# Kernel tuning notes

Measured on AMD Instinct MI355X. Metric: run time of the kernel, lower is better.

The kernel has to match this reference:

```python
import jax, jax.numpy as jnp
import numpy as np

B, S, SE, D, H, FF, E, K = 2, 2048, 2048, 1024, 16, 4096, 8, 2
HD = D // H


def setup_inputs() -> dict:
    key = jax.random.key(0)
    ks = jax.random.split(key, 32)
    w = lambda k, shape: jax.random.normal(k, shape, jnp.float32) * 0.02
    inp = {
        'x': jax.random.normal(ks[0], (B, S, D), jnp.float32),
        'encoder_output': jax.random.normal(ks[1], (B, SE, D), jnp.float32),
        # causal self-attention projections
        'sa_wq': w(ks[2], (D, D)), 'sa_bq': jnp.zeros((D,), jnp.float32),
        'sa_wk': w(ks[3], (D, D)), 'sa_bk': jnp.zeros((D,), jnp.float32),
        'sa_wv': w(ks[4], (D, D)), 'sa_bv': jnp.zeros((D,), jnp.float32),
        'sa_wo': w(ks[5], (D, D)), 'sa_bo': jnp.zeros((D,), jnp.float32),
        # cross-attention projections
        'ca_wq': w(ks[6], (D, D)), 'ca_bq': jnp.zeros((D,), jnp.float32),
        'ca_wk': w(ks[7], (D, D)), 'ca_bk': jnp.zeros((D,), jnp.float32),
        'ca_wv': w(ks[8], (D, D)), 'ca_bv': jnp.zeros((D,), jnp.float32),
        'ca_wo': w(ks[9], (D, D)), 'ca_bo': jnp.zeros((D,), jnp.float32),
        # layernorms
        'ln1_g': jnp.ones((D,), jnp.float32), 'ln1_b': jnp.zeros((D,), jnp.float32),
        'ln2_g': jnp.ones((D,), jnp.float32), 'ln2_b': jnp.zeros((D,), jnp.float32),
        'ln3_g': jnp.ones((D,), jnp.float32), 'ln3_b': jnp.zeros((D,), jnp.float32),
        # router + experts
        'router_w': w(ks[10], (D, E)), 'router_b': jnp.zeros((E,), jnp.float32),
        'e_w1': w(ks[11], (E, D, FF)), 'e_b1': jnp.zeros((E, FF), jnp.float32),
        'e_w2': w(ks[12], (E, FF, D)), 'e_b2': jnp.zeros((E, D), jnp.float32),
    }
    return inp


def _layernorm(x, g, b):
    m = x.mean(-1, keepdims=True)
    v = ((x - m) ** 2).mean(-1, keepdims=True)
    return (x - m) / jnp.sqrt(v + 1e-5) * g + b


def _attn(q_in, k_in, v_in, wq, bq, wk, bk, wv, bv, wo, bo, causal):
    Bq, Sq, Dm = q_in.shape
    Sk = k_in.shape[1]
    Q = (q_in @ wq + bq).reshape(Bq, Sq, H, HD)
    Kp = (k_in @ wk + bk).reshape(Bq, Sk, H, HD)
    V = (v_in @ wv + bv).reshape(Bq, Sk, H, HD)
    scores = jnp.einsum('bqhd,bkhd->bhqk', Q, Kp) / jnp.sqrt(jnp.float32(HD))
    if causal:
        mask = jnp.tril(jnp.ones((Sq, Sk), bool))
        scores = jnp.where(mask, scores, -jnp.inf)
    a = jax.nn.softmax(scores, axis=-1)
    o = jnp.einsum('bhqk,bkhd->bqhd', a, V).reshape(Bq, Sq, Dm)
    return o @ wo + bo


def _moe(x, rw, rb, w1, b1, w2, b2):
    T = x.shape[0] * x.shape[1]
    xf = x.reshape(T, D)
    router_weights = jax.nn.softmax(xf @ rw + rb, axis=-1)          # [T,E]
    topw, topi = jax.lax.top_k(router_weights, K)                   # [T,K]
    topw = jax.nn.softmax(topw, axis=-1)                            # renormalize top-k
    # combine[t,e] = sum_k topw[t,k] * (topi[t,k]==e)
    combine = jnp.zeros((T, E), xf.dtype).at[jnp.arange(T)[:, None], topi].add(topw)
    # dense compute over all experts (same math as masked dispatch)
    h = jax.nn.gelu(jnp.einsum('td,edf->etf', xf, w1) + b1[:, None, :], approximate=False)
    eo = jnp.einsum('etf,efd->etd', h, w2) + b2[:, None, :]          # [E,T,D]
    out = jnp.einsum('etd,te->td', eo, combine)
    return out.reshape(x.shape)


def reference(x, encoder_output,
              sa_wq, sa_bq, sa_wk, sa_bk, sa_wv, sa_bv, sa_wo, sa_bo,
              ca_wq, ca_bq, ca_wk, ca_bk, ca_wv, ca_bv, ca_wo, ca_bo,
              ln1_g, ln1_b, ln2_g, ln2_b, ln3_g, ln3_b,
              router_w, router_b, e_w1, e_b1, e_w2, e_b2):
    x = _layernorm(x + _attn(x, x, x, sa_wq, sa_bq, sa_wk, sa_bk, sa_wv, sa_bv, sa_wo, sa_bo, True), ln1_g, ln1_b)
    x = _layernorm(x + _attn(x, encoder_output, encoder_output, ca_wq, ca_bq, ca_wk, ca_bk, ca_wv, ca_bv, ca_wo, ca_bo, False), ln2_g, ln2_b)
    x = _layernorm(x + _moe(x, router_w, router_b, e_w1, e_b1, e_w2, e_b2), ln3_g, ln3_b)
    return x
```

## Files before the change

kernel.cpp:

```cpp
#include <hip/hip_runtime.h>

typedef unsigned short u16;
typedef unsigned int   u32;
typedef __bf16    bf16x8 __attribute__((ext_vector_type(8)));
typedef _Float16  f16x8  __attribute__((ext_vector_type(8)));
typedef _Float16  f16x4  __attribute__((ext_vector_type(4)));
typedef __fp16    fp16x2 __attribute__((ext_vector_type(2)));
typedef float     f32x4  __attribute__((ext_vector_type(4)));
typedef u16       u16x4  __attribute__((ext_vector_type(4)));

#define DEV static __device__ __forceinline__

#if __has_builtin(__builtin_amdgcn_mfma_f32_16x16x16f16)
#define HAVE_MFMA16 1
#else
#define HAVE_MFMA16 0
#endif

constexpr int DIMc  = 1024;
constexpr int NHEAD = 16;
constexpr int HDM   = 64;
constexpr int SLENc = 2048;
constexpr int NBAT  = 2;
constexpr int NTOK  = NBAT * SLENc;
constexpr int FFD   = 4096;
constexpr int NEXP  = 8;
constexpr int NSLOT = 2 * NTOK;
constexpr long TD   = (long)NTOK * DIMc;
constexpr float RSC = 2048.0f;
constexpr float RSCI = 1.0f / 2048.0f;

DEV u16 f2bf(float f) {
  u32 u = __float_as_uint(f);
  u += 0x7fffu + ((u >> 16) & 1u);
  return (u16)(u >> 16);
}
DEV float bf2f(u16 h) { return __uint_as_float(((u32)h) << 16); }
DEV float h2f(u16 u) { union { _Float16 h; u16 u_; } x; x.u_ = u; return (float)x.h; }

DEV void split2v(float v, u16& h, u16& r) {
  _Float16 hh = (_Float16)v;
  float rf = (v - (float)hh) * RSC;
  union { _Float16 h_; u16 u_; } a, b;
  a.h_ = hh; b.h_ = (_Float16)rf;
  h = a.u_; r = b.u_;
}

DEV u32 pkrtz(float a, float b) {
  union { fp16x2 v; u32 u; } x;
  x.v = __builtin_amdgcn_cvt_pkrtz(a, b);
  return x.u;
}

DEV f16x4 mk4(u32 lo, u32 hi) {
  union { u32 u[2]; f16x4 v; } x;
  x.u[0] = lo; x.u[1] = hi;
  return x.v;
}

DEV void async16(const void* g, void* l) {
  __builtin_amdgcn_global_load_lds((const u32*)g, (u32*)l, 16, 0, 0);
}

DEV f32x4 mfma_bf(bf16x8 a, bf16x8 b, f32x4 c) {
  return __builtin_amdgcn_mfma_f32_16x16x32_bf16(a, b, c, 0, 0, 0);
}
DEV f32x4 mfma_h(f16x8 a, f16x8 b, f32x4 c) {
  return __builtin_amdgcn_mfma_f32_16x16x32_f16(a, b, c, 0, 0, 0);
}
#if HAVE_MFMA16
DEV f32x4 mfma16h(f16x4 a, f16x4 b, f32x4 c) {
  return __builtin_amdgcn_mfma_f32_16x16x16f16(a, b, c, 0, 0, 0);
}
#endif

DEV f16x8 ldfragh(const u16 (*T)[64], int row, int blk) {
  return *(const f16x8*)((const u16*)T + row * 64 + ((blk ^ (row & 7)) * 8));
}
DEV f16x4 ldVfrag4(const u16 (*T)[64], int row, int kn, int kc) {
  const int blk = kn * 2 + (kc >> 1);
  const u16* p = (const u16*)T + row * 64 + ((blk ^ (row & 7)) * 8) + (kc & 1) * 4;
  return *(const f16x4*)p;
}

DEV float gelu_fast(float v) {
  float arg = v * fmaf(0.044715f * v, v, 1.0f) * 0.7978845608028654f;
  return v / (1.0f + __expf(-2.0f * arg));
}

__global__ __launch_bounds__(256) void split2_kernel(
    const float* __restrict__ x, u16* __restrict__ o0, u16* __restrict__ o1, long n) {
  long i = ((long)blockIdx.x * 256 + threadIdx.x) * 4;
  if (i >= n) return;
  f32x4 v = *(const f32x4*)(x + i);
  u16x4 h, r;
#pragma unroll
  for (int j = 0; j < 4; ++j) { u16 a, b; split2v(v[j], a, b); h[j] = a; r[j] = b; }
  *(u16x4*)(o0 + i) = h;
  *(u16x4*)(o1 + i) = r;
}

__global__ __launch_bounds__(256) void wsplit2_kernel(
    const float* __restrict__ W, u16* __restrict__ t0, u16* __restrict__ t1, int R, int C) {
  __shared__ alignas(16) float tile[32][33];
  const long base = (long)blockIdx.z * R * C;
  const int c0 = blockIdx.x * 32, r0 = blockIdx.y * 32;
  const int tx = threadIdx.x & 31, ty = threadIdx.x >> 5;
#pragma unroll
  for (int i = 0; i < 32; i += 8)
    tile[ty + i][tx] = W[base + (long)(r0 + ty + i) * C + (c0 + tx)];
  __syncthreads();
#pragma unroll
  for (int i = 0; i < 32; i += 8) {
    float v = tile[tx][ty + i];
    long oidx = base + (long)(c0 + ty + i) * R + (r0 + tx);
    u16 a, b; split2v(v, a, b);
    t0[oidx] = a; t1[oidx] = b;
  }
}

__global__ __launch_bounds__(256) void wsplit1_kernel(
    const float* __restrict__ W, u16* __restrict__ t0, int R, int C) {
  __shared__ alignas(16) float tile[32][33];
  const long base = (long)blockIdx.z * R * C;
  const int c0 = blockIdx.x * 32, r0 = blockIdx.y * 32;
  const int tx = threadIdx.x & 31, ty = threadIdx.x >> 5;
#pragma unroll
  for (int i = 0; i < 32; i += 8)
    tile[ty + i][tx] = W[base + (long)(r0 + ty + i) * C + (c0 + tx)];
  __syncthreads();
#pragma unroll
  for (int i = 0; i < 32; i += 8) {
    long oidx = base + (long)(c0 + ty + i) * R + (r0 + tx);
    t0[oidx] = f2bf(tile[tx][ty + i]);
  }
}

__global__ __launch_bounds__(256) void biascat_kernel(
    const float* __restrict__ q, const float* __restrict__ k, const float* __restrict__ v,
    const float* __restrict__ ck, const float* __restrict__ cv,
    float* __restrict__ qkvb, float* __restrict__ kvb) {
  int i = blockIdx.x * 256 + threadIdx.x;
  if (i < 1024) qkvb[i] = q[i];
  else if (i < 2048) qkvb[i] = k[i - 1024];
  else if (i < 3072) qkvb[i] = v[i - 2048];
  else if (i < 4096) kvb[i - 3072] = ck[i - 3072];
  else if (i < 5120) kvb[i - 3072] = cv[i - 4096];
}

__global__ __launch_bounds__(256) void vtrans2_kernel(
    const u16* __restrict__ vh, const u16* __restrict__ vr, int ld,
    u16* __restrict__ t0, u16* __restrict__ t1) {
  __shared__ alignas(16) float tile[32][33];
  const int bh = blockIdx.z, b = bh >> 4, h = bh & 15;
  const int s0 = blockIdx.x * 32, d0 = blockIdx.y * 32;
  const int tx = threadIdx.x & 31, ty = threadIdx.x >> 5;
#pragma unroll
  for (int i = 0; i < 32; i += 8) {
    long idx = (long)(b * SLENc + s0 + ty + i) * ld + h * HDM + d0 + tx;
    tile[ty + i][tx] = h2f(vh[idx]) + h2f(vr[idx]) * RSCI;
  }
  __syncthreads();
#pragma unroll
  for (int i = 0; i < 32; i += 8) {
    float v = tile[tx][ty + i];
    long o = ((long)bh * HDM + d0 + ty + i) * SLENc + s0 + tx;
    u16 a, b_; split2v(v, a, b_);
    t0[o] = a; t1[o] = b_;
  }
}

template<int MT, int BK, bool SPLIT, bool GATHER, int EPI>
__global__ __launch_bounds__(256) void gemm_kernel(
    const u16* __restrict__ A0, const u16* __restrict__ A1,
    const u16* __restrict__ B0, const u16* __restrict__ B1,
    const float* __restrict__ bias, void* __restrict__ Cout, u16* __restrict__ C1,
    int M, int N, int Kd,
    const int* __restrict__ tlist, const int* __restrict__ cnts, const int* __restrict__ offs) {
  constexpr int NP   = SPLIT ? 2 : 1;
  constexpr int RPC  = 512 / BK;
  constexpr int ACH  = (MT / RPC) / 4;
  constexpr int BCH  = (128 / RPC) / 4;
  constexpr int MREP = MT / 32;
  constexpr int WRS  = MT / 2;
  __shared__ alignas(16) u16 As[NP][MT * BK];
  __shared__ alignas(16) u16 Bs[NP][128 * BK];

  const int e   = blockIdx.z;
  const int cnt = cnts ? cnts[e] : M;
  const int off = offs ? offs[e] : 0;
  const int m0  = blockIdx.y * MT;
  if (m0 >= cnt) return;
  const int n0  = blockIdx.x * 128;

  const int tid = threadIdx.x;
  const int lane = tid & 63, wid = tid >> 6;
  const int fr = lane & 15, kc = lane >> 4;
  const int wr = wid >> 1, wc = wid & 1;

  const long boff = (long)e * N * Kd;

  int srow, kseg8;
  if constexpr (BK == 32) { srow = lane >> 2; kseg8 = lane & 3; }
  else                    { srow = lane >> 3; kseg8 = (lane & 7) ^ (srow & 7); }

  long aoff[ACH], boff_[BCH];
#pragma unroll
  for (int c = 0; c < ACH; ++c) {
    const int row = (wid * ACH + c) * RPC + srow;
    long ar;
    if (GATHER) {
      int idx = m0 + row; if (idx >= cnt) idx = cnt - 1;
      ar = tlist[off + idx];
    } else {
      ar = (long)(off + m0 + row);
    }
    aoff[c] = ar * Kd + kseg8 * 8;
  }
#pragma unroll
  for (int c = 0; c < BCH; ++c) {
    const int row = (wid * BCH + c) * RPC + srow;
    boff_[c] = boff + (long)(n0 + row) * Kd + kseg8 * 8;
  }

  f32x4 acc[MREP][4], acc1[MREP][4];
#pragma unroll
  for (int m = 0; m < MREP; ++m)
#pragma unroll
    for (int n = 0; n < 4; ++n) { acc[m][n] = f32x4{0.f,0.f,0.f,0.f}; acc1[m][n] = f32x4{0.f,0.f,0.f,0.f}; }

  const int NK = Kd / BK;
  for (int kt = 0; kt < NK; ++kt) {
    const int k0 = kt * BK;
    __syncthreads();
#pragma unroll
    for (int c = 0; c < ACH; ++c) {
      const int chunk = wid * ACH + c;
      async16(A0 + aoff[c] + k0, &As[0][chunk * 512]);
      if constexpr (SPLIT) async16(A1 + aoff[c] + k0, &As[1][chunk * 512]);
    }
#pragma unroll
    for (int c = 0; c < BCH; ++c) {
      const int chunk = wid * BCH + c;
      async16(B0 + boff_[c] + k0, &Bs[0][chunk * 512]);
      if constexpr (SPLIT) async16(B1 + boff_[c] + k0, &Bs[1][chunk * 512]);
    }
    __syncthreads();

    if constexpr (BK == 32) {
      if constexpr (SPLIT) {
        f16x8 a0[MREP], a1[MREP];
#pragma unroll
        for (int m = 0; m < MREP; ++m) {
          const int idx = (wr * WRS + m * 16 + fr) * 32 + kc * 8;
          a0[m] = *(const f16x8*)&As[0][idx];
          a1[m] = *(const f16x8*)&As[1][idx];
        }
#pragma unroll
        for (int n = 0; n < 4; ++n) {
          const int idx = (wc * 64 + n * 16 + fr) * 32 + kc * 8;
          f16x8 b0 = *(const f16x8*)&Bs[0][idx];
          f16x8 b1 = *(const f16x8*)&Bs[1][idx];
#pragma unroll
          for (int m = 0; m < MREP; ++m) {
            acc[m][n]  = mfma_h(a0[m], b0, acc[m][n]);
            acc1[m][n] = mfma_h(a0[m], b1, acc1[m][n]);
            acc1[m][n] = mfma_h(a1[m], b0, acc1[m][n]);
          }
        }
      } else {
        bf16x8 a0[MREP];
#pragma unroll
        for (int m = 0; m < MREP; ++m)
          a0[m] = *(const bf16x8*)&As[0][(wr * WRS + m * 16 + fr) * 32 + kc * 8];
#pragma unroll
        for (int n = 0; n < 4; ++n) {
          bf16x8 b0 = *(const bf16x8*)&Bs[0][(wc * 64 + n * 16 + fr) * 32 + kc * 8];
#pragma unroll
          for (int m = 0; m < MREP; ++m)
            acc[m][n] = mfma_bf(a0[m], b0, acc[m][n]);
        }
      }
    } else {
#pragma unroll
      for (int ksub = 0; ksub < 2; ++ksub) {
        bf16x8 a0[MREP];
#pragma unroll
        for (int m = 0; m < MREP; ++m) {
          const int row = wr * WRS + m * 16 + fr;
          a0[m] = *(const bf16x8*)&As[0][row * 64 + (((ksub << 2) | kc) ^ (fr & 7)) * 8];
        }
#pragma unroll
        for (int n = 0; n < 4; ++n) {
          const int row = wc * 64 + n * 16 + fr;
          bf16x8 b0 = *(const bf16x8*)&Bs[0][row * 64 + (((ksub << 2) | kc) ^ (fr & 7)) * 8];
#pragma unroll
          for (int m = 0; m < MREP; ++m)
            acc[m][n] = mfma_bf(a0[m], b0, acc[m][n]);
        }
      }
    }
  }

  const float* bvec = bias + (long)e * N;
#pragma unroll
  for (int m = 0; m < MREP; ++m) {
#pragma unroll
    for (int j = 0; j < 4; ++j) {
      const int r = m0 + wr * WRS + m * 16 + kc * 4 + j;
      if (r >= cnt) continue;
      const long orow = (long)(off + r) * N;
#pragma unroll
      for (int n = 0; n < 4; ++n) {
        const int col = n0 + wc * 64 + n * 16 + fr;
        float v = acc[m][n][j];
        if constexpr (SPLIT) v += acc1[m][n][j] * RSCI;
        v += bvec[col];
        if constexpr (EPI == 0) {
          ((float*)Cout)[orow + col] = v;
        } else if constexpr (EPI == 1) {
          ((u16*)Cout)[orow + col] = f2bf(gelu_fast(v));
        } else if constexpr (EPI == 2) {
          ((u16*)Cout)[orow + col] = f2bf(v);
        } else {
          u16 a_, b_; split2v(v, a_, b_);
          ((u16*)Cout)[orow + col] = a_;
          C1[orow + col] = b_;
        }
      }
    }
  }
}

#if !HAVE_MFMA16
DEV f16x8 gather_fragh(u32 a0, u32 a1, u32 b0, u32 b1, int lane) {
  const int kc = lane >> 4;
  const int base = (lane & 15) + ((kc & 1) << 5);
  union { u32 u[4]; f16x8 v; } r;
  u32 s00 = (u32)__shfl((int)a0, base, 64);
  u32 s01 = (u32)__shfl((int)a1, base, 64);
  u32 s10 = (u32)__shfl((int)b0, base, 64);
  u32 s11 = (u32)__shfl((int)b1, base, 64);
  u32 t00 = (u32)__shfl((int)a0, base + 16, 64);
  u32 t01 = (u32)__shfl((int)a1, base + 16, 64);
  u32 t10 = (u32)__shfl((int)b0, base + 16, 64);
  u32 t11 = (u32)__shfl((int)b1, base + 16, 64);
  const bool hi = (kc >> 1) != 0;
  r.u[0] = hi ? s10 : s00;
  r.u[1] = hi ? s11 : s01;
  r.u[2] = hi ? t10 : t00;
  r.u[3] = hi ? t11 : t01;
  return r.v;
}
#endif

template<bool CAUSAL>
__global__ __launch_bounds__(256, 3) void attn2_kernel(
    const u16* __restrict__ Qh, const u16* __restrict__ Qr, int qld,
    const u16* __restrict__ Kh, const u16* __restrict__ Kr, int kld,
    const u16* __restrict__ Vh, const u16* __restrict__ Vr,
    u16* __restrict__ OH, u16* __restrict__ OR) {
  __shared__ alignas(16) u16 KQs[2][64][64];
  __shared__ alignas(16) u16 Vts[2][64][64];

  const int qt = CAUSAL ? ((int)gridDim.x - 1 - (int)blockIdx.x) : (int)blockIdx.x;
  const int h = blockIdx.y, b = blockIdx.z;
  const int tid = threadIdx.x, lane = tid & 63, w = tid >> 6;
  const int fr = lane & 15, kc = lane >> 4;
  const int q0 = qt * 64;
  const long qbase = (long)(b * SLENc) * qld + h * HDM;
  const long kbase = (long)(b * SLENc) * kld + h * HDM;
  const long obase = (long)(b * SLENc) * DIMc + h * HDM;
  const long vtbase = (long)(b * NHEAD + h) * HDM * SLENc;
  const int r = lane >> 3, blk = (lane & 7) ^ r;

#pragma unroll
  for (int p = 0; p < 2; ++p) {
    const u16* gp = (p == 0 ? Qh : Qr);
#pragma unroll
    for (int cc = 0; cc < 2; ++cc) {
      int c = w + 4 * cc;
      async16(gp + qbase + (long)(q0 + 8 * c + r) * qld + blk * 8, &KQs[p][8 * c][0]);
    }
  }
  __syncthreads();
  f16x8 qf0[2], qf1[2];
#pragma unroll
  for (int s = 0; s < 2; ++s) {
    qf0[s] = ldfragh(KQs[0], w * 16 + fr, s * 4 + kc);
    qf1[s] = ldfragh(KQs[1], w * 16 + fr, s * 4 + kc);
  }
  __syncthreads();

  f32x4 accO0[4], accO1[4];
#pragma unroll
  for (int dn = 0; dn < 4; ++dn) { accO0[dn] = f32x4{0.f,0.f,0.f,0.f}; accO1[dn] = f32x4{0.f,0.f,0.f,0.f}; }
  float m_ = -3e38f, l_ = 0.f;

  const int nkt = CAUSAL ? (qt + 1) : (SLENc / 64);
  for (int kt = 0; kt < nkt; ++kt) {
    __syncthreads();
    {
#pragma unroll
      for (int p = 0; p < 2; ++p) {
        const u16* gp = (p == 0 ? Kh : Kr);
#pragma unroll
        for (int cc = 0; cc < 2; ++cc) {
          int c = w + 4 * cc;
          async16(gp + kbase + (long)(kt * 64 + 8 * c + r) * kld + blk * 8, &KQs[p][8 * c][0]);
        }
      }
      const long vrow = vtbase + kt * 64;
#pragma unroll
      for (int p = 0; p < 2; ++p) {
        const u16* gp = (p == 0 ? Vh : Vr);
#pragma unroll
        for (int cc = 0; cc < 2; ++cc) {
          int c = w + 4 * cc;
          async16(gp + vrow + (long)(8 * c + r) * SLENc + blk * 8, &Vts[p][8 * c][0]);
        }
      }
    }
    __syncthreads();

    f32x4 sc0[4], sc1[4];
#pragma unroll
    for (int kn = 0; kn < 4; ++kn) { sc0[kn] = f32x4{0.f,0.f,0.f,0.f}; sc1[kn] = f32x4{0.f,0.f,0.f,0.f}; }
    __builtin_amdgcn_s_setprio(1);
#pragma unroll
    for (int kn = 0; kn < 4; ++kn)
#pragma unroll
      for (int s = 0; s < 2; ++s) {
        f16x8 ah = ldfragh(KQs[0], kn * 16 + fr, s * 4 + kc);
        f16x8 ar = ldfragh(KQs[1], kn * 16 + fr, s * 4 + kc);
        sc0[kn] = mfma_h(ah, qf0[s], sc0[kn]);
        sc1[kn] = mfma_h(ah, qf1[s], sc1[kn]);
        sc1[kn] = mfma_h(ar, qf0[s], sc1[kn]);
      }
    __builtin_amdgcn_s_setprio(0);

    constexpr float SCL = 0.125f, SCL2 = 0.125f * RSCI;
    float p_[4][4];
    float mx = -3e38f;
#pragma unroll
    for (int kn = 0; kn < 4; ++kn)
#pragma unroll
      for (int j = 0; j < 4; ++j) {
        float sv = fmaf(sc0[kn][j], SCL, sc1[kn][j] * SCL2);
        if (CAUSAL && kt == qt) {
          if (kn * 16 + kc * 4 + j > w * 16 + fr) sv = -3e38f;
        }
        p_[kn][j] = sv;
        mx = fmaxf(mx, sv);
      }
    mx = fmaxf(mx, __shfl_xor(mx, 16, 64));
    mx = fmaxf(mx, __shfl_xor(mx, 32, 64));
    if (!__all(mx <= m_ + 8.f)) {
      const float mn = fmaxf(m_, mx);
      const float corr = __expf(m_ - mn);
      m_ = mn;
      l_ *= corr;
#pragma unroll
      for (int dn = 0; dn < 4; ++dn) { accO0[dn] *= corr; accO1[dn] *= corr; }
    }
    float rs = 0.f;
#pragma unroll
    for (int kn = 0; kn < 4; ++kn)
#pragma unroll
      for (int j = 0; j < 4; ++j) {
        float p = __expf(p_[kn][j] - m_);
        p_[kn][j] = p;
        rs += p;
      }
    rs += __shfl_xor(rs, 16, 64);
    rs += __shfl_xor(rs, 32, 64);
    l_ += rs;

#if HAVE_MFMA16
#pragma unroll
    for (int kn = 0; kn < 4; ++kn) {
      u32 hp0 = pkrtz(p_[kn][0], p_[kn][1]);
      u32 hp1 = pkrtz(p_[kn][2], p_[kn][3]);
      float h0 = h2f((u16)hp0), h1 = h2f((u16)(hp0 >> 16));
      float h2_ = h2f((u16)hp1), h3 = h2f((u16)(hp1 >> 16));
      u32 rp0 = pkrtz((p_[kn][0] - h0) * RSC, (p_[kn][1] - h1) * RSC);
      u32 rp1 = pkrtz((p_[kn][2] - h2_) * RSC, (p_[kn][3] - h3) * RSC);
      f16x4 ph = mk4(hp0, hp1), pr = mk4(rp0, rp1);
      __builtin_amdgcn_s_setprio(1);
#pragma unroll
      for (int dn = 0; dn < 4; ++dn) {
        f16x4 vh = ldVfrag4(Vts[0], dn * 16 + fr, kn, kc);
        f16x4 vr = ldVfrag4(Vts[1], dn * 16 + fr, kn, kc);
        accO0[dn] = mfma16h(vh, ph, accO0[dn]);
        accO1[dn] = mfma16h(vh, pr, accO1[dn]);
        accO1[dn] = mfma16h(vr, ph, accO1[dn]);
      }
      __builtin_amdgcn_s_setprio(0);
    }
#else
    u32 hpk[4][2], rpk[4][2];
#pragma unroll
    for (int kn = 0; kn < 4; ++kn)
#pragma unroll
      for (int jp = 0; jp < 2; ++jp) {
        float p0 = p_[kn][2 * jp], p1 = p_[kn][2 * jp + 1];
        u32 hp = pkrtz(p0, p1);
        float h0 = h2f((u16)hp), h1 = h2f((u16)(hp >> 16));
        u32 rp = pkrtz((p0 - h0) * RSC, (p1 - h1) * RSC);
        hpk[kn][jp] = hp;
        rpk[kn][jp] = rp;
      }
#pragma unroll
    for (int s = 0; s < 2; ++s) {
      f16x8 ph = gather_fragh(hpk[2 * s][0], hpk[2 * s][1], hpk[2 * s + 1][0], hpk[2 * s + 1][1], lane);
      f16x8 pr = gather_fragh(rpk[2 * s][0], rpk[2 * s][1], rpk[2 * s + 1][0], rpk[2 * s + 1][1], lane);
      __builtin_amdgcn_s_setprio(1);
#pragma unroll
      for (int dn = 0; dn < 4; ++dn) {
        f16x8 vh = ldfragh(Vts[0], dn * 16 + fr, s * 4 + kc);
        f16x8 vr = ldfragh(Vts[1], dn * 16 + fr, s * 4 + kc);
        accO0[dn] = mfma_h(vh, ph, accO0[dn]);
        accO1[dn] = mfma_h(vh, pr, accO1[dn]);
        accO1[dn] = mfma_h(vr, ph, accO1[dn]);
      }
      __builtin_amdgcn_s_setprio(0);
    }
#endif
  }

  const float inv = 1.0f / l_;
#pragma unroll
  for (int dn = 0; dn < 4; ++dn) {
    u16x4 hv, rv;
#pragma unroll
    for (int j = 0; j < 4; ++j) {
      float o = (accO0[dn][j] + accO1[dn][j] * RSCI) * inv;
      u16 a_, b_; split2v(o, a_, b_);
      hv[j] = a_; rv[j] = b_;
    }
    const long oidx = obase + (long)(q0 + w * 16 + fr) * DIMc + dn * 16 + kc * 4;
    *(u16x4*)&OH[oidx] = hv;
    *(u16x4*)&OR[oidx] = rv;
  }
}

template<int NS>
__global__ __launch_bounds__(256) void resln_kernel(
    const float* __restrict__ resid, const float* __restrict__ proj,
    const float* __restrict__ gam, const float* __restrict__ bet,
    float* __restrict__ yout, u16* __restrict__ s0, u16* __restrict__ s1) {
  __shared__ float red[4];
  const int t = blockIdx.x, tid = threadIdx.x;
  const long base = (long)t * DIMc;
  float v[4];
#pragma unroll
  for (int i = 0; i < 4; ++i) {
    int d = tid + i * 256;
    v[i] = resid[base + d] + proj[base + d];
  }
  float s = v[0] + v[1] + v[2] + v[3];
#pragma unroll
  for (int o = 32; o; o >>= 1) s += __shfl_xor(s, o, 64);
  if ((tid & 63) == 0) red[tid >> 6] = s;
  __syncthreads();
  const float mean = (red[0] + red[1] + red[2] + red[3]) * (1.0f / DIMc);
  __syncthreads();
  float q = 0.f;
#pragma unroll
  for (int i = 0; i < 4; ++i) { float d_ = v[i] - mean; q += d_ * d_; }
#pragma unroll
  for (int o = 32; o; o >>= 1) q += __shfl_xor(q, o, 64);
  if ((tid & 63) == 0) red[tid >> 6] = q;
  __syncthreads();
  const float var = (red[0] + red[1] + red[2] + red[3]) * (1.0f / DIMc);
  const float inv = rsqrtf(var + 1e-5f);
#pragma unroll
  for (int i = 0; i < 4; ++i) {
    int d = tid + i * 256;
    float y = (v[i] - mean) * inv * gam[d] + bet[d];
    yout[base + d] = y;
    if constexpr (NS == 1) s0[base + d] = f2bf(y);
    if constexpr (NS == 2) {
      u16 a, b; split2v(y, a, b);
      s0[base + d] = a; s1[base + d] = b;
    }
  }
}

__global__ __launch_bounds__(256) void resln_router_kernel(
    const float* __restrict__ resid, const float* __restrict__ proj,
    const float* __restrict__ gam, const float* __restrict__ bet,
    const float* __restrict__ rw, const float* __restrict__ rb,
    float* __restrict__ yout, u16* __restrict__ s0,
    int* __restrict__ topi, float* __restrict__ topw, int* __restrict__ cnt) {
  __shared__ float red[4];
  __shared__ float rpart[4][8];
  const int t = blockIdx.x, tid = threadIdx.x;
  const int lane = tid & 63, wv = tid >> 6;
  const long base = (long)t * DIMc;
  float v[4];
#pragma unroll
  for (int i = 0; i < 4; ++i) {
    int d = tid + i * 256;
    v[i] = resid[base + d] + proj[base + d];
  }
  float s = v[0] + v[1] + v[2] + v[3];
#pragma unroll
  for (int o = 32; o; o >>= 1) s += __shfl_xor(s, o, 64);
  if (lane == 0) red[wv] = s;
  __syncthreads();
  const float mean = (red[0] + red[1] + red[2] + red[3]) * (1.0f / DIMc);
  __syncthreads();
  float q = 0.f;
#pragma unroll
  for (int i = 0; i < 4; ++i) { float d_ = v[i] - mean; q += d_ * d_; }
#pragma unroll
  for (int o = 32; o; o >>= 1) q += __shfl_xor(q, o, 64);
  if (lane == 0) red[wv] = q;
  __syncthreads();
  const float var = (red[0] + red[1] + red[2] + red[3]) * (1.0f / DIMc);
  const float inv = rsqrtf(var + 1e-5f);
  float part[8] = {};
#pragma unroll
  for (int i = 0; i < 4; ++i) {
    int d = tid + i * 256;
    float y = (v[i] - mean) * inv * gam[d] + bet[d];
    yout[base + d] = y;
    s0[base + d] = f2bf(y);
    const f32x4* wp = (const f32x4*)&rw[d * 8];
    f32x4 w0 = wp[0], w1 = wp[1];
    part[0] += y * w0[0]; part[1] += y * w0[1]; part[2] += y * w0[2]; part[3] += y * w0[3];
    part[4] += y * w1[0]; part[5] += y * w1[1]; part[6] += y * w1[2]; part[7] += y * w1[3];
  }
#pragma unroll
  for (int o = 32; o; o >>= 1)
#pragma unroll
    for (int e = 0; e < 8; ++e) part[e] += __shfl_xor(part[e], o, 64);
  if (lane == 0)
#pragma unroll
    for (int e = 0; e < 8; ++e) rpart[wv][e] = part[e];
  __syncthreads();
  if (tid == 0) {
    float lg[8];
#pragma unroll
    for (int e = 0; e < 8; ++e)
      lg[e] = rpart[0][e] + rpart[1][e] + rpart[2][e] + rpart[3][e] + rb[e];
    int i1 = 0;
#pragma unroll
    for (int e = 1; e < 8; ++e) if (lg[e] > lg[i1]) i1 = e;
    int i2 = (i1 == 0) ? 1 : 0;
#pragma unroll
    for (int e = 0; e < 8; ++e) if (e != i1 && lg[e] > lg[i2]) i2 = e;
    float mx = lg[i1], ps = 0.f, p[8];
#pragma unroll
    for (int e = 0; e < 8; ++e) { p[e] = __expf(lg[e] - mx); ps += p[e]; }
    float p1 = p[i1] / ps, p2 = p[i2] / ps;
    float e2 = __expf(p2 - p1);
    float w1 = 1.0f / (1.0f + e2);
    topi[t * 2] = i1; topi[t * 2 + 1] = i2;
    topw[t * 2] = w1; topw[t * 2 + 1] = e2 * w1;
    atomicAdd(&cnt[i1], 1); atomicAdd(&cnt[i2], 1);
  }
}

__global__ void scan_kernel(const int* __restrict__ cnt, int* __restrict__ offs, int* __restrict__ pos) {
  if (threadIdx.x == 0) {
    int a = 0;
    for (int e = 0; e < NEXP; ++e) { offs[e] = a; a += cnt[e]; }
  }
  if (threadIdx.x < NEXP) pos[threadIdx.x] = 0;
}

__global__ __launch_bounds__(256) void fill_kernel(
    const int* __restrict__ topi, const int* __restrict__ offs, int* __restrict__ pos,
    int* __restrict__ tlist, int* __restrict__ slotof) {
  int t = blockIdx.x * 256 + threadIdx.x;
  if (t >= NTOK) return;
#pragma unroll
  for (int k = 0; k < 2; ++k) {
    int e = topi[t * 2 + k];
    int pp = atomicAdd(&pos[e], 1);
    int s = offs[e] + pp;
    tlist[s] = t;
    slotof[t * 2 + k] = s;
  }
}

__global__ __launch_bounds__(256) void final_kernel(
    const float* __restrict__ x2, const u16* __restrict__ eo,
    const int* __restrict__ slotof, const float* __restrict__ topw,
    const float* __restrict__ gam, const float* __restrict__ bet, float* __restrict__ out) {
  __shared__ float red[4];
  const int t = blockIdx.x, tid = threadIdx.x;
  const long base = (long)t * DIMc;
  const int s0 = slotof[t * 2], s1 = slotof[t * 2 + 1];
  const float w0 = topw[t * 2], w1 = topw[t * 2 + 1];
  float v[4];
#pragma unroll
  for (int i = 0; i < 4; ++i) {
    int d = tid + i * 256;
    float moe = w0 * bf2f(eo[(long)s0 * DIMc + d]) + w1 * bf2f(eo[(long)s1 * DIMc + d]);
    v[i] = x2[base + d] + moe;
  }
  float s = v[0] + v[1] + v[2] + v[3];
#pragma unroll
  for (int o = 32; o; o >>= 1) s += __shfl_xor(s, o, 64);
  if ((tid & 63) == 0) red[tid >> 6] = s;
  __syncthreads();
  const float mean = (red[0] + red[1] + red[2] + red[3]) * (1.0f / DIMc);
  __syncthreads();
  float q = 0.f;
#pragma unroll
  for (int i = 0; i < 4; ++i) { float d_ = v[i] - mean; q += d_ * d_; }
#pragma unroll
  for (int o = 32; o; o >>= 1) q += __shfl_xor(q, o, 64);
  if ((tid & 63) == 0) red[tid >> 6] = q;
  __syncthreads();
  const float var = (red[0] + red[1] + red[2] + red[3]) * (1.0f / DIMc);
  const float inv = rsqrtf(var + 1e-5f);
#pragma unroll
  for (int i = 0; i < 4; ++i) {
    int d = tid + i * 256;
    out[base + d] = (v[i] - mean) * inv * gam[d] + bet[d];
  }
}

extern "C" void kernel_launch(void* const* d_in, const int* in_sizes, int n_in,
                              void* d_out, int out_size, void* d_ws, size_t ws_size,
                              hipStream_t stream) {
  (void)in_sizes; (void)n_in; (void)out_size; (void)ws_size;
  const float* x     = (const float*)d_in[0];
  const float* enc   = (const float*)d_in[1];
  const float* aw[8] = {(const float*)d_in[2],  (const float*)d_in[4],  (const float*)d_in[6],  (const float*)d_in[8],
                        (const float*)d_in[10], (const float*)d_in[12], (const float*)d_in[14], (const float*)d_in[16]};
  const float* ab[8] = {(const float*)d_in[3],  (const float*)d_in[5],  (const float*)d_in[7],  (const float*)d_in[9],
                        (const float*)d_in[11], (const float*)d_in[13], (const float*)d_in[15], (const float*)d_in[17]};
  const float* ln1_g = (const float*)d_in[18]; const float* ln1_b = (const float*)d_in[19];
  const float* ln2_g = (const float*)d_in[20]; const float* ln2_b = (const float*)d_in[21];
  const float* ln3_g = (const float*)d_in[22]; const float* ln3_b = (const float*)d_in[23];
  const float* rw    = (const float*)d_in[24]; const float* rb    = (const float*)d_in[25];
  const float* e_w1  = (const float*)d_in[26]; const float* e_b1  = (const float*)d_in[27];
  const float* e_w2  = (const float*)d_in[28]; const float* e_b2  = (const float*)d_in[29];

  char* basep = (char*)d_ws;
  size_t offb = 0;
  auto alloc = [&](size_t nbytes) -> void* {
    void* r = basep + offb;
    offb += (nbytes + 255) & ~(size_t)255;
    return r;
  };

  const size_t PLANE_BF = (size_t)TD * 2;
  const size_t PLANE_F  = (size_t)TD * 4;
  const size_t WPLANE   = (size_t)DIMc * DIMc * 2;

  u16 *xs0 = (u16*)alloc(PLANE_BF), *xs1 = (u16*)alloc(PLANE_BF);
  u16 *es0 = (u16*)alloc(PLANE_BF), *es1 = (u16*)alloc(PLANE_BF);
  u16 *os0 = (u16*)alloc(PLANE_BF), *os1 = (u16*)alloc(PLANE_BF);
  u16 *wqkv0 = (u16*)alloc(3 * WPLANE), *wqkv1 = (u16*)alloc(3 * WPLANE);
  u16 *wkv0  = (u16*)alloc(2 * WPLANE), *wkv1  = (u16*)alloc(2 * WPLANE);
  u16 *wq0   = (u16*)alloc(WPLANE),     *wq1   = (u16*)alloc(WPLANE);
  u16 *wo10  = (u16*)alloc(WPLANE),     *wo11  = (u16*)alloc(WPLANE);
  u16 *wo20  = (u16*)alloc(WPLANE),     *wo21  = (u16*)alloc(WPLANE);
  u16* w1t = (u16*)alloc((size_t)NEXP * FFD * DIMc * 2);
  u16* w2t = (u16*)alloc((size_t)NEXP * DIMc * FFD * 2);
  u16 *QKVh = (u16*)alloc(3 * PLANE_BF), *QKVr = (u16*)alloc(3 * PLANE_BF);
  u16 *KVh  = (u16*)alloc(2 * PLANE_BF), *KVr  = (u16*)alloc(2 * PLANE_BF);
  u16 *Qch  = (u16*)alloc(PLANE_BF),     *Qcr  = (u16*)alloc(PLANE_BF);
  u16 *Vth  = (u16*)alloc(PLANE_BF),     *Vtr  = (u16*)alloc(PLANE_BF);
  float* qkvb = (float*)alloc(3072 * 4);
  float* kvb  = (float*)alloc(2048 * 4);
  float* aout = (float*)alloc(PLANE_F);
  float* x1   = (float*)alloc(PLANE_F);
  float* x2   = (float*)alloc(PLANE_F);
  u16*   x2h  = (u16*)alloc(PLANE_BF);
  u16*   hbuf = (u16*)alloc((size_t)(NSLOT + 128) * FFD * 2);
  u16*   eo   = (u16*)alloc((size_t)NSLOT * DIMc * 2);
  int*   topi   = (int*)alloc(NSLOT * 4);
  float* topwp  = (float*)alloc(NSLOT * 4);
  int*   tlist  = (int*)alloc(NSLOT * 4);
  int*   slotof = (int*)alloc(NSLOT * 4);
  int*   cnt    = (int*)alloc(NEXP * 4);
  int*   offs   = (int*)alloc(NEXP * 4);
  int*   pos    = (int*)alloc(NEXP * 4);

  (void)hipMemsetAsync(cnt, 0, NEXP * sizeof(int), stream);

  const int SB = (int)(TD / 4 / 256);
  split2_kernel<<<SB, 256, 0, stream>>>(x, xs0, xs1, TD);
  split2_kernel<<<SB, 256, 0, stream>>>(enc, es0, es1, TD);
  for (int s = 0; s < 3; ++s)
    wsplit2_kernel<<<dim3(32, 32, 1), 256, 0, stream>>>(aw[s], wqkv0 + (size_t)s * DIMc * DIMc, wqkv1 + (size_t)s * DIMc * DIMc, DIMc, DIMc);
  wsplit2_kernel<<<dim3(32, 32, 1), 256, 0, stream>>>(aw[5], wkv0, wkv1, DIMc, DIMc);
  wsplit2_kernel<<<dim3(32, 32, 1), 256, 0, stream>>>(aw[6], wkv0 + (size_t)DIMc * DIMc, wkv1 + (size_t)DIMc * DIMc, DIMc, DIMc);
  wsplit2_kernel<<<dim3(32, 32, 1), 256, 0, stream>>>(aw[4], wq0, wq1, DIMc, DIMc);
  wsplit2_kernel<<<dim3(32, 32, 1), 256, 0, stream>>>(aw[3], wo10, wo11, DIMc, DIMc);
  wsplit2_kernel<<<dim3(32, 32, 1), 256, 0, stream>>>(aw[7], wo20, wo21, DIMc, DIMc);
  wsplit1_kernel<<<dim3(FFD / 32, DIMc / 32, NEXP), 256, 0, stream>>>(e_w1, w1t, DIMc, FFD);
  wsplit1_kernel<<<dim3(DIMc / 32, FFD / 32, NEXP), 256, 0, stream>>>(e_w2, w2t, FFD, DIMc);
  biascat_kernel<<<20, 256, 0, stream>>>(ab[0], ab[1], ab[2], ab[5], ab[6], qkvb, kvb);

  const dim3 gproj(DIMc / 128, NTOK / 64, 1);
  const dim3 gqkv(3 * DIMc / 128, NTOK / 64, 1);
  const dim3 gkv(2 * DIMc / 128, NTOK / 64, 1);
  const dim3 gattn(SLENc / 64, NHEAD, NBAT);
  const dim3 gvt(SLENc / 32, HDM / 32, NBAT * NHEAD);

  gemm_kernel<64, 32, true, false, 3><<<gqkv, 256, 0, stream>>>(xs0, xs1, wqkv0, wqkv1, qkvb, QKVh, QKVr, NTOK, 3 * DIMc, DIMc, nullptr, nullptr, nullptr);
  vtrans2_kernel<<<gvt, 256, 0, stream>>>(QKVh + 2048, QKVr + 2048, 3 * DIMc, Vth, Vtr);
  attn2_kernel<true><<<gattn, 256, 0, stream>>>(QKVh, QKVr, 3 * DIMc, QKVh + 1024, QKVr + 1024, 3 * DIMc, Vth, Vtr, os0, os1);
  gemm_kernel<64, 32, true, false, 0><<<gproj, 256, 0, stream>>>(os0, os1, wo10, wo11, ab[3], aout, nullptr, NTOK, DIMc, DIMc, nullptr, nullptr, nullptr);
  resln_kernel<2><<<NTOK, 256, 0, stream>>>(x, aout, ln1_g, ln1_b, x1, xs0, xs1);
  gemm_kernel<64, 32, true, false, 3><<<gproj, 256, 0, stream>>>(xs0, xs1, wq0, wq1, ab[4], Qch, Qcr, NTOK, DIMc, DIMc, nullptr, nullptr, nullptr);
  gemm_kernel<64, 32, true, false, 3><<<gkv, 256, 0, stream>>>(es0, es1, wkv0, wkv1, kvb, KVh, KVr, NTOK, 2 * DIMc, DIMc, nullptr, nullptr, nullptr);
  vtrans2_kernel<<<gvt, 256, 0, stream>>>(KVh + 1024, KVr + 1024, 2 * DIMc, Vth, Vtr);
  attn2_kernel<false><<<gattn, 256, 0, stream>>>(Qch, Qcr, DIMc, KVh, KVr, 2 * DIMc, Vth, Vtr, os0, os1);
  gemm_kernel<64, 32, true, false, 0><<<gproj, 256, 0, stream>>>(os0, os1, wo20, wo21, ab[7], aout, nullptr, NTOK, DIMc, DIMc, nullptr, nullptr, nullptr);
  resln_router_kernel<<<NTOK, 256, 0, stream>>>(x1, aout, ln2_g, ln2_b, rw, rb, x2, x2h, topi, topwp, cnt);
  scan_kernel<<<1, 64, 0, stream>>>(cnt, offs, pos);
  fill_kernel<<<NTOK / 256, 256, 0, stream>>>(topi, offs, pos, tlist, slotof);
  gemm_kernel<128, 64, false, true, 1><<<dim3(FFD / 128, NTOK / 128, NEXP), 256, 0, stream>>>(
      x2h, nullptr, w1t, nullptr, e_b1, hbuf, nullptr, NTOK, FFD, DIMc, tlist, cnt, offs);
  gemm_kernel<128, 64, false, false, 2><<<dim3(DIMc / 128, NTOK / 128, NEXP), 256, 0, stream>>>(
      hbuf, nullptr, w2t, nullptr, e_b2, eo, nullptr, NTOK, DIMc, FFD, nullptr, cnt, offs);
  final_kernel<<<NTOK, 256, 0, stream>>>(x2, eo, slotof, topwp, ln3_g, ln3_b, (float*)d_out);
}
```

Before: 1.201 ms.

## Double-buffer shared-memory tiles in GEMM and attention to overlap loads with MFMA

The BK=32 GEMM path and the attention kernel now use two shared-memory buffers. The next K/V (or A/B) tile is issued asynchronously right after the barrier, and the MFMA work runs on the current buffer, removing one barrier per iteration and hiding global-load latency behind compute. The cost is double the LDS footprint in the attention kernel, whose launch bound drops from 3 to 2 blocks per CU, and more LDS in the GEMM. That can reduce occupancy.

After: 1.187 ms. About the same (-1.2%).

```diff
diff --git a/kernel.cpp b/kernel.cpp
--- a/kernel.cpp
+++ b/kernel.cpp
@@ -178,13 +178,14 @@
     int M, int N, int Kd,
     const int* __restrict__ tlist, const int* __restrict__ cnts, const int* __restrict__ offs) {
   constexpr int NP   = SPLIT ? 2 : 1;
+  constexpr int NBUF = (BK == 32) ? 2 : 1;
   constexpr int RPC  = 512 / BK;
   constexpr int ACH  = (MT / RPC) / 4;
   constexpr int BCH  = (128 / RPC) / 4;
   constexpr int MREP = MT / 32;
   constexpr int WRS  = MT / 2;
-  __shared__ alignas(16) u16 As[NP][MT * BK];
-  __shared__ alignas(16) u16 Bs[NP][128 * BK];
+  __shared__ alignas(16) u16 As[NBUF][NP][MT * BK];
+  __shared__ alignas(16) u16 Bs[NBUF][NP][128 * BK];
 
   const int e   = blockIdx.z;
   const int cnt = cnts ? cnts[e] : M;
@@ -229,38 +230,37 @@
 #pragma unroll
     for (int n = 0; n < 4; ++n) { acc[m][n] = f32x4{0.f,0.f,0.f,0.f}; acc1[m][n] = f32x4{0.f,0.f,0.f,0.f}; }
 
-  const int NK = Kd / BK;
-  for (int kt = 0; kt < NK; ++kt) {
+  auto stage = [&](int kt, int bufi) {
     const int k0 = kt * BK;
-    __syncthreads();
 #pragma unroll
     for (int c = 0; c < ACH; ++c) {
       const int chunk = wid * ACH + c;
-      async16(A0 + aoff[c] + k0, &As[0][chunk * 512]);
-      if constexpr (SPLIT) async16(A1 + aoff[c] + k0, &As[1][chunk * 512]);
+      async16(A0 + aoff[c] + k0, &As[bufi][0][chunk * 512]);
+      if constexpr (SPLIT) async16(A1 + aoff[c] + k0, &As[bufi][1][chunk * 512]);
     }
 #pragma unroll
     for (int c = 0; c < BCH; ++c) {
       const int chunk = wid * BCH + c;
-      async16(B0 + boff_[c] + k0, &Bs[0][chunk * 512]);
-      if constexpr (SPLIT) async16(B1 + boff_[c] + k0, &Bs[1][chunk * 512]);
-    }
-    __syncthreads();
-
+      async16(B0 + boff_[c] + k0, &Bs[bufi][0][chunk * 512]);
+      if constexpr (SPLIT) async16(B1 + boff_[c] + k0, &Bs[bufi][1][chunk * 512]);
+    }
+  };
+
+  auto compute = [&](int bufi) {
     if constexpr (BK == 32) {
       if constexpr (SPLIT) {
         f16x8 a0[MREP], a1[MREP];
 #pragma unroll
         for (int m = 0; m < MREP; ++m) {
           const int idx = (wr * WRS + m * 16 + fr) * 32 + kc * 8;
-          a0[m] = *(const f16x8*)&As[0][idx];
-          a1[m] = *(const f16x8*)&As[1][idx];
+          a0[m] = *(const f16x8*)&As[bufi][0][idx];
+          a1[m] = *(const f16x8*)&As[bufi][1][idx];
         }
 #pragma unroll
         for (int n = 0; n < 4; ++n) {
           const int idx = (wc * 64 + n * 16 + fr) * 32 + kc * 8;
-          f16x8 b0 = *(const f16x8*)&Bs[0][idx];
-          f16x8 b1 = *(const f16x8*)&Bs[1][idx];
+          f16x8 b0 = *(const f16x8*)&Bs[bufi][0][idx];
+          f16x8 b1 = *(const f16x8*)&Bs[bufi][1][idx];
 #pragma unroll
           for (int m = 0; m < MREP; ++m) {
             acc[m][n]  = mfma_h(a0[m], b0, acc[m][n]);
@@ -272,10 +272,10 @@
         bf16x8 a0[MREP];
 #pragma unroll
         for (int m = 0; m < MREP; ++m)
-          a0[m] = *(const bf16x8*)&As[0][(wr * WRS + m * 16 + fr) * 32 + kc * 8];
+          a0[m] = *(const bf16x8*)&As[bufi][0][(wr * WRS + m * 16 + fr) * 32 + kc * 8];
 #pragma unroll
         for (int n = 0; n < 4; ++n) {
-          bf16x8 b0 = *(const bf16x8*)&Bs[0][(wc * 64 + n * 16 + fr) * 32 + kc * 8];
+          bf16x8 b0 = *(const bf16x8*)&Bs[bufi][0][(wc * 64 + n * 16 + fr) * 32 + kc * 8];
 #pragma unroll
           for (int m = 0; m < MREP; ++m)
             acc[m][n] = mfma_bf(a0[m], b0, acc[m][n]);
@@ -288,17 +288,36 @@
 #pragma unroll
         for (int m = 0; m < MREP; ++m) {
           const int row = wr * WRS + m * 16 + fr;
-          a0[m] = *(const bf16x8*)&As[0][row * 64 + (((ksub << 2) | kc) ^ (fr & 7)) * 8];
+          a0[m] = *(const bf16x8*)&As[0][0][row * 64 + (((ksub << 2) | kc) ^ (fr & 7)) * 8];
         }
 #pragma unroll
         for (int n = 0; n < 4; ++n) {
           const int row = wc * 64 + n * 16 + fr;
-          bf16x8 b0 = *(const bf16x8*)&Bs[0][row * 64 + (((ksub << 2) | kc) ^ (fr & 7)) * 8];
+          bf16x8 b0 = *(const bf16x8*)&Bs[0][0][row * 64 + (((ksub << 2) | kc) ^ (fr & 7)) * 8];
 #pragma unroll
           for (int m = 0; m < MREP; ++m)
             acc[m][n] = mfma_bf(a0[m], b0, acc[m][n]);
         }
       }
+    }
+  };
+
+  const int NK = Kd / BK;
+  if constexpr (BK == 32) {
+    stage(0, 0);
+    int cur = 0;
+    for (int kt = 0; kt < NK; ++kt) {
+      __syncthreads();
+      if (kt + 1 < NK) stage(kt + 1, cur ^ 1);
+      compute(cur);
+      cur ^= 1;
+    }
+  } else {
+    for (int kt = 0; kt < NK; ++kt) {
+      __syncthreads();
+      stage(kt, 0);
+      __syncthreads();
+      compute(0);
     }
   }
 
@@ -355,13 +374,13 @@
 #endif
 
 template<bool CAUSAL>
-__global__ __launch_bounds__(256, 3) void attn2_kernel(
+__global__ __launch_bounds__(256, 2) void attn2_kernel(
     const u16* __restrict__ Qh, const u16* __restrict__ Qr, int qld,
     const u16* __restrict__ Kh, const u16* __restrict__ Kr, int kld,
     const u16* __restrict__ Vh, const u16* __restrict__ Vr,
     u16* __restrict__ OH, u16* __restrict__ OR) {
-  __shared__ alignas(16) u16 KQs[2][64][64];
-  __shared__ alignas(16) u16 Vts[2][64][64];
+  __shared__ alignas(16) u16 KQs[2][2][64][64];
+  __shared__ alignas(16) u16 Vts[2][2][64][64];
 
   const int qt = CAUSAL ? ((int)gridDim.x - 1 - (int)blockIdx.x) : (int)blockIdx.x;
   const int h = blockIdx.y, b = blockIdx.z;
@@ -374,23 +393,45 @@
   const long vtbase = (long)(b * NHEAD + h) * HDM * SLENc;
   const int r = lane >> 3, blk = (lane & 7) ^ r;
 
+  auto stageKV = [&](int kt, int bufi) {
+#pragma unroll
+    for (int p = 0; p < 2; ++p) {
+      const u16* gp = (p == 0 ? Kh : Kr);
+#pragma unroll
+      for (int cc = 0; cc < 2; ++cc) {
+        int c = w + 4 * cc;
+        async16(gp + kbase + (long)(kt * 64 + 8 * c + r) * kld + blk * 8, &KQs[bufi][p][8 * c][0]);
+      }
+    }
+    const long vrow = vtbase + kt * 64;
+#pragma unroll
+    for (int p = 0; p < 2; ++p) {
+      const u16* gp = (p == 0 ? Vh : Vr);
+#pragma unroll
+      for (int cc = 0; cc < 2; ++cc) {
+        int c = w + 4 * cc;
+        async16(gp + vrow + (long)(8 * c + r) * SLENc + blk * 8, &Vts[bufi][p][8 * c][0]);
+      }
+    }
+  };
+
 #pragma unroll
   for (int p = 0; p < 2; ++p) {
     const u16* gp = (p == 0 ? Qh : Qr);
 #pragma unroll
     for (int cc = 0; cc < 2; ++cc) {
       int c = w + 4 * cc;
-      async16(gp + qbase + (long)(q0 + 8 * c + r) * qld + blk * 8, &KQs[p][8 * c][0]);
+      async16(gp + qbase + (long)(q0 + 8 * c + r) * qld + blk * 8, &KQs[0][p][8 * c][0]);
     }
   }
   __syncthreads();
   f16x8 qf0[2], qf1[2];
 #pragma unroll
   for (int s = 0; s < 2; ++s) {
-    qf0[s] = ldfragh(KQs[0], w * 16 + fr, s * 4 + kc);
-    qf1[s] = ldfragh(KQs[1], w * 16 + fr, s * 4 + kc);
-  }
-  __syncthreads();
+    qf0[s] = ldfragh(KQs[0][0], w * 16 + fr, s * 4 + kc);
+    qf1[s] = ldfragh(KQs[0][1], w * 16 + fr, s * 4 + kc);
+  }
+  stageKV(0, 1);
 
   f32x4 accO0[4], accO1[4];
 #pragma unroll
@@ -398,30 +439,10 @@
   float m_ = -3e38f, l_ = 0.f;
 
   const int nkt = CAUSAL ? (qt + 1) : (SLENc / 64);
+  int cur = 1;
   for (int kt = 0; kt < nkt; ++kt) {
     __syncthreads();
-    {
-#pragma unroll
-      for (int p = 0; p < 2; ++p) {
-        const u16* gp = (p == 0 ? Kh : Kr);
-#pragma unroll
-        for (int cc = 0; cc < 2; ++cc) {
-          int c = w + 4 * cc;
-          async16(gp + kbase + (long)(kt * 64 + 8 * c + r) * kld + blk * 8, &KQs[p][8 * c][0]);
-        }
-      }
-      const long vrow = vtbase + kt * 64;
-#pragma unroll
-      for (int p = 0; p < 2; ++p) {
-        const u16* gp = (p == 0 ? Vh : Vr);
-#pragma unroll
-        for (int cc = 0; cc < 2; ++cc) {
-          int c = w + 4 * cc;
-          async16(gp + vrow + (long)(8 * c + r) * SLENc + blk * 8, &Vts[p][8 * c][0]);
-        }
-      }
-    }
-    __syncthreads();
+    if (kt + 1 < nkt) stageKV(kt + 1, cur ^ 1);
 
     f32x4 sc0[4], sc1[4];
 #pragma unroll
@@ -431,8 +452,8 @@
     for (int kn = 0; kn < 4; ++kn)
 #pragma unroll
       for (int s = 0; s < 2; ++s) {
-        f16x8 ah = ldfragh(KQs[0], kn * 16 + fr, s * 4 + kc);
-        f16x8 ar = ldfragh(KQs[1], kn * 16 + fr, s * 4 + kc);
+        f16x8 ah = ldfragh(KQs[cur][0], kn * 16 + fr, s * 4 + kc);
+        f16x8 ar = ldfragh(KQs[cur][1], kn * 16 + fr, s * 4 + kc);
         sc0[kn] = mfma_h(ah, qf0[s], sc0[kn]);
         sc1[kn] = mfma_h(ah, qf1[s], sc1[kn]);
         sc1[kn] = mfma_h(ar, qf0[s], sc1[kn]);
@@ -489,8 +510,8 @@
       __builtin_amdgcn_s_setprio(1);
 #pragma unroll
       for (int dn = 0; dn < 4; ++dn) {
-        f16x4 vh = ldVfrag4(Vts[0], dn * 16 + fr, kn, kc);
-        f16x4 vr = ldVfrag4(Vts[1], dn * 16 + fr, kn, kc);
+        f16x4 vh = ldVfrag4(Vts[cur][0], dn * 16 + fr, kn, kc);
+        f16x4 vr = ldVfrag4(Vts[cur][1], dn * 16 + fr, kn, kc);
         accO0[dn] = mfma16h(vh, ph, accO0[dn]);
         accO1[dn] = mfma16h(vh, pr, accO1[dn]);
         accO1[dn] = mfma16h(vr, ph, accO1[dn]);
@@ -517,8 +538,8 @@
       __builtin_amdgcn_s_setprio(1);
 #pragma unroll
       for (int dn = 0; dn < 4; ++dn) {
-        f16x8 vh = ldfragh(Vts[0], dn * 16 + fr, s * 4 + kc);
-        f16x8 vr = ldfragh(Vts[1], dn * 16 + fr, s * 4 + kc);
+        f16x8 vh = ldfragh(Vts[cur][0], dn * 16 + fr, s * 4 + kc);
+        f16x8 vr = ldfragh(Vts[cur][1], dn * 16 + fr, s * 4 + kc);
         accO0[dn] = mfma_h(vh, ph, accO0[dn]);
         accO1[dn] = mfma_h(vh, pr, accO1[dn]);
         accO1[dn] = mfma_h(vr, ph, accO1[dn]);
@@ -526,6 +547,7 @@
       __builtin_amdgcn_s_setprio(0);
     }
 #endif
+    cur ^= 1;
   }
 
   const float inv = 1.0f / l_;
```
